# Optimization experiments

Measured on AMD Instinct MI355X. Metric: run time of the kernel, lower is better.

Reference implementation:

```python
import jax, jax.numpy as jnp
import numpy as np

B, C, H, W = 8, 3, 64, 64
HORIZON = 32
WIDTH = 32
M1 = M2 = M3 = 8
N_LAYERS = 4
C_OUT = 3


def setup_inputs() -> dict:
    key = jax.random.key(0)
    ks = jax.random.split(key, 16)
    scale = 1.0 / (WIDTH * WIDTH)
    wshape = (N_LAYERS, 4, WIDTH, WIDTH, M1, M2, M3)
    return {
        "x_t": jax.random.normal(ks[0], (B, C, H, W), dtype=jnp.float32),
        "p_w": jax.random.normal(ks[1], (WIDTH, C + 3), dtype=jnp.float32) * 0.1,
        "p_b": jnp.zeros((WIDTH,), dtype=jnp.float32),
        "spec_wr": scale * jax.random.normal(ks[2], wshape, dtype=jnp.float32),
        "spec_wi": scale * jax.random.normal(ks[3], wshape, dtype=jnp.float32),
        "pw_w": jax.random.normal(ks[4], (N_LAYERS, WIDTH, WIDTH), dtype=jnp.float32) * 0.1,
        "pw_b": jnp.zeros((N_LAYERS, WIDTH), dtype=jnp.float32),
        "q1_w": jax.random.normal(ks[5], (2 * WIDTH, WIDTH), dtype=jnp.float32) * 0.1,
        "q1_b": jnp.zeros((2 * WIDTH,), dtype=jnp.float32),
        "q2_w": jax.random.normal(ks[6], (C_OUT, 2 * WIDTH), dtype=jnp.float32) * 0.1,
        "q2_b": jnp.zeros((C_OUT,), dtype=jnp.float32),
        "horizon": HORIZON,
    }


def _conv1x1(x, w, b):
    # x: [b, i, x, y, z], w: [o, i] -> [b, o, x, y, z]
    return jnp.einsum("oi,bixyz->boxyz", w, x) + b[None, :, None, None, None]


def _spectral_conv3d(x, wr, wi):
    # x: [b, i, H, W, T]; wr/wi: [4, i, o, m1, m2, m3]
    h, w_, t = x.shape[-3], x.shape[-2], x.shape[-1]
    xf = jnp.fft.rfftn(x, axes=(-3, -2, -1))  # [b, i, H, W, T//2+1]
    wc = (wr + 1j * wi).astype(xf.dtype)
    m1 = min(M1, xf.shape[-3]); m2 = min(M2, xf.shape[-2]); m3 = min(M3, xf.shape[-1])
    mul = lambda a, ww: jnp.einsum("bixyz,ioxyz->boxyz", a, ww)
    out = jnp.zeros((x.shape[0], wr.shape[2]) + xf.shape[2:], dtype=xf.dtype)
    out = out.at[:, :, :m1, :m2, :m3].set(mul(xf[:, :, :m1, :m2, :m3], wc[0, :, :, :m1, :m2, :m3]))
    out = out.at[:, :, -m1:, :m2, :m3].set(mul(xf[:, :, -m1:, :m2, :m3], wc[1, :, :, :m1, :m2, :m3]))
    out = out.at[:, :, :m1, -m2:, :m3].set(mul(xf[:, :, :m1, -m2:, :m3], wc[2, :, :, :m1, :m2, :m3]))
    out = out.at[:, :, -m1:, -m2:, :m3].set(mul(xf[:, :, -m1:, -m2:, :m3], wc[3, :, :, :m1, :m2, :m3]))
    return jnp.fft.irfftn(out, s=(h, w_, t), axes=(-3, -2, -1))


def _grid_3d(b, h, w, t, dtype):
    gy = jnp.broadcast_to(jnp.linspace(0.0, 1.0, h, dtype=dtype)[None, None, :, None, None], (b, 1, h, w, t))
    gx = jnp.broadcast_to(jnp.linspace(0.0, 1.0, w, dtype=dtype)[None, None, None, :, None], (b, 1, h, w, t))
    gt = jnp.broadcast_to(jnp.linspace(0.0, 1.0, t, dtype=dtype)[None, None, None, None, :], (b, 1, h, w, t))
    return jnp.concatenate([gy, gx, gt], axis=1)


def reference(x_t, p_w, p_b, spec_wr, spec_wi, pw_w, pw_b, q1_w, q1_b, q2_w, q2_b, horizon):
    b, c, h, w = x_t.shape
    x = jnp.broadcast_to(x_t[..., None], (b, c, h, w, horizon))  # repeat over time
    grid = _grid_3d(b, h, w, horizon, x_t.dtype)
    x = jnp.concatenate([x, grid], axis=1)  # [b, c+3, h, w, t]
    x = _conv1x1(x, p_w, p_b)
    for l in range(N_LAYERS):
        x = jax.nn.gelu(
            _spectral_conv3d(x, spec_wr[l], spec_wi[l]) + _conv1x1(x, pw_w[l], pw_b[l]),
            approximate=False,
        )
    x = _conv1x1(x, q1_w, q1_b)
    x = jax.nn.gelu(x, approximate=False)
    x = _conv1x1(x, q2_w, q2_b)
    # [b, c_out, h, w, t] -> [b, t, c_out, h, w]
    return jnp.transpose(x, (0, 4, 1, 2, 3))
```

## Files before the change

### kernel.cpp

```cpp
#include <hip/hip_runtime.h>
#include <math.h>


#define TWO_PI 6.2831853071795864769f

typedef short bf16x8 __attribute__((ext_vector_type(8)));
typedef float f32x4 __attribute__((ext_vector_type(4)));
typedef float v2f __attribute__((ext_vector_type(2)));

__device__ __forceinline__ f32x4 mfma16(bf16x8 a, bf16x8 b, f32x4 c) {
    return __builtin_amdgcn_mfma_f32_16x16x32_bf16(a, b, c, 0, 0, 0);
}

__device__ __forceinline__ void split8(float4 a, float4 b, bf16x8& h, bf16x8& l) {
    float f[8] = {a.x, a.y, a.z, a.w, b.x, b.y, b.z, b.w};
    #pragma unroll
    for (int i = 0; i < 8; ++i) {
        unsigned u = __float_as_uint(f[i]);
        h[i] = (short)(u >> 16);
        float hf = __uint_as_float(u & 0xFFFF0000u);
        float lf = f[i] - hf;
        l[i] = (short)(__float_as_uint(lf) >> 16);
    }
}

__device__ __forceinline__ unsigned packhl(float f) {
    unsigned u = __float_as_uint(f);
    unsigned hi = u & 0xFFFF0000u;
    float lf = f - __uint_as_float(hi);
    return hi | (__float_as_uint(lf) >> 16);
}

__device__ __forceinline__ void unpack8(uint4 a, uint4 b, bf16x8& h, bf16x8& l) {
    unsigned u[8] = {a.x, a.y, a.z, a.w, b.x, b.y, b.z, b.w};
    #pragma unroll
    for (int i = 0; i < 8; ++i) {
        h[i] = (short)(u[i] >> 16);
        l[i] = (short)(u[i] & 0xFFFFu);
    }
}

__device__ __forceinline__ v2f make2(float x) { v2f r; r.x = x; r.y = x; return r; }
__device__ __forceinline__ v2f fma2(v2f a, v2f b, v2f c) { return __builtin_elementwise_fma(a, b, c); }

__device__ __forceinline__ v2f gelu2(v2f v) {
    v2f u = v * 0.70710678118654752f;
    v2f a = __builtin_elementwise_abs(u);
    v2f den = fma2(a, make2(0.3275911f), make2(1.0f));
    v2f t; t.x = __builtin_amdgcn_rcpf(den.x); t.y = __builtin_amdgcn_rcpf(den.y);
    v2f p = t * (0.254829592f + t * (-0.284496736f + t * (1.421413741f +
            t * (-1.453152027f + t * 1.061405429f))));
    v2f e; e.x = __expf(-u.x * u.x); e.y = __expf(-u.y * u.y);
    v2f m = fma2(-p, e, make2(1.0f));
    v2f erfu = __builtin_elementwise_copysign(m, u);
    return 0.5f * v * (1.0f + erfu);
}

__device__ __forceinline__ void gelu4(f32x4& q) {
    v2f p0; p0.x = q[0]; p0.y = q[1];
    v2f p1; p1.x = q[2]; p1.y = q[3];
    p0 = gelu2(p0); p1 = gelu2(p1);
    q[0] = p0.x; q[1] = p0.y; q[2] = p1.x; q[3] = p1.y;
}

__device__ __forceinline__ void make_fwd_A(int l15, int quad, bf16x8& Gh, bf16x8& Gl) {
    int k = l15 >> 1;
    float s0, c0, ds, dc;
    __sincosf((float)(k * quad * 8) * (TWO_PI / 32.0f), &s0, &c0);
    __sincosf((float)k * (TWO_PI / 32.0f), &ds, &dc);
    float m[8];
    float cc = c0, ss = s0;
    #pragma unroll
    for (int j = 0; j < 8; ++j) {
        m[j] = (l15 & 1) ? -ss : cc;
        float nc = cc * dc - ss * ds;
        float ns = ss * dc + cc * ds;
        cc = nc; ss = ns;
    }
    split8(make_float4(m[0], m[1], m[2], m[3]),
           make_float4(m[4], m[5], m[6], m[7]), Gh, Gl);
}

__device__ __forceinline__ void fwd_tdft(const unsigned* up, int b, int sp0,
                                         float2* __restrict__ T1,
                                         int wb, int l15, int quad,
                                         bf16x8 Gh, bf16x8 Gl) {
    #pragma unroll
    for (int nt = 0; nt < 4; ++nt) {
        int r = wb + nt * 16 + l15;
        const uint4* p = (const uint4*)(up + r * 36 + quad * 8);
        bf16x8 bh, bl; unpack8(p[0], p[1], bh, bl);
        f32x4 d = {0.f, 0.f, 0.f, 0.f};
        d = mfma16(Gh, bh, d);
        d = mfma16(Gl, bh, d);
        d = mfma16(Gh, bl, d);
        int c = r & 31, spl = r >> 5;
        float4* ob = (float4*)(T1 + ((long)(b * 32 + c) * 4096 + sp0 + spl) * 8 + quad * 2);
        *ob = make_float4(d[0], d[1], d[2], d[3]);
    }
}

__global__ __launch_bounds__(256) void k_lift(const float* __restrict__ xt,
                                              const float* __restrict__ pw,
                                              const float* __restrict__ pb,
                                              float* __restrict__ X,
                                              float2* __restrict__ T1) {
    __shared__ unsigned xs[9216];
    int g = blockIdx.x;
    int spt = g & 511, b = g >> 9;
    int sp0 = spt * 8;
    int y = sp0 >> 6, x0 = sp0 & 63;
    int tid = threadIdx.x;
    int t = tid & 31, spl = tid >> 5;
    int sp = sp0 + spl;
    float a0 = xt[(b * 3 + 0) * 4096 + sp];
    float a1 = xt[(b * 3 + 1) * 4096 + sp];
    float a2 = xt[(b * 3 + 2) * 4096 + sp];
    float gy = y * (1.0f / 63.0f), gx = (x0 + spl) * (1.0f / 63.0f), gt = t * (1.0f / 31.0f);
    float v[32];
    #pragma unroll
    for (int c = 0; c < 32; ++c) {
        const float* w = pw + c * 6;
        v[c] = pb[c] + w[0] * a0 + w[1] * a1 + w[2] * a2
             + w[3] * gy + w[4] * gx + w[5] * gt;
    }
    float* xg = X + (((long)(b * 4096 + sp)) * 32 + t) * 32;
    #pragma unroll
    for (int j = 0; j < 8; ++j)
        ((float4*)xg)[j] = make_float4(v[4*j], v[4*j+1], v[4*j+2], v[4*j+3]);
    #pragma unroll
    for (int c = 0; c < 32; ++c)
        xs[(spl * 32 + c) * 36 + t] = packhl(v[c]);
    int wave = tid >> 6, lane = tid & 63, l15 = lane & 15, quad = lane >> 4;
    bf16x8 Gh, Gl; make_fwd_A(l15, quad, Gh, Gl);
    __syncthreads();
    fwd_tdft(xs, b, sp0, T1, wave * 64, l15, quad, Gh, Gl);
}

__global__ __launch_bounds__(256) void k_xdft(const float2* __restrict__ T1, float2* __restrict__ T2) {
    __shared__ float2 s[1024];
    __shared__ float2 tw[64];
    int g = blockIdx.x;
    int ypair = g & 31; int bc = g >> 5;
    long base = ((long)bc * 64 + ypair * 2) * 512;
    int tid = threadIdx.x;
    for (int k = tid; k < 1024; k += 256) s[k] = T1[base + k];
    if (tid < 64) { float sn, cs; __sincosf(tid * (TWO_PI / 64.0f), &sn, &cs); tw[tid] = make_float2(cs, sn); }
    __syncthreads();
    #pragma unroll
    for (int r = 0; r < 2; ++r) {
        int j = tid + r * 256;
        int half = j >> 8, rem = j & 255;
        int idx = half * 512 + rem;
        float2 a = s[idx], b2 = s[idx + 256];
        s[idx] = make_float2(a.x + b2.x, a.y + b2.y);
        s[idx + 256] = make_float2(a.x - b2.x, a.y - b2.y);
    }
    __syncthreads();
    int half = tid >> 7, jj = tid & 127;
    int kxi = jj >> 3, kt = jj & 7;
    int kx = kxi < 8 ? kxi : kxi + 48;
    const float2* row = s + half * 512 + (kx & 1) * 256;
    float sr = 0.f, si = 0.f;
    for (int x = 0; x < 32; ++x) {
        float2 w = tw[(kx * x) & 63];
        float2 a = row[x * 8 + kt];
        sr += a.x * w.x + a.y * w.y;
        si += a.y * w.x - a.x * w.y;
    }
    T2[((long)bc * 64 + ypair * 2 + half) * 128 + jj] = make_float2(sr, si);
}

__global__ __launch_bounds__(128) void k_ydft(const float2* __restrict__ T2, float2* __restrict__ T3) {
    __shared__ float2 s[512];
    __shared__ float2 tw[64];
    int g = blockIdx.x;
    int kx = g & 15; int bc = g >> 4;
    int tid = threadIdx.x;
    for (int k = tid; k < 512; k += 128) {
        int y = k >> 3, kt = k & 7;
        s[k] = T2[((long)bc * 64 + y) * 128 + kx * 8 + kt];
    }
    if (tid < 64) { float sn, cs; __sincosf(tid * (TWO_PI / 64.0f), &sn, &cs); tw[tid] = make_float2(cs, sn); }
    __syncthreads();
    #pragma unroll
    for (int r = 0; r < 2; ++r) {
        int j = tid + r * 128;
        float2 a = s[j], b2 = s[j + 256];
        s[j] = make_float2(a.x + b2.x, a.y + b2.y);
        s[j + 256] = make_float2(a.x - b2.x, a.y - b2.y);
    }
    __syncthreads();
    int kyi = tid >> 3, kt = tid & 7;
    int ky = kyi < 8 ? kyi : kyi + 48;
    const float2* row = s + (ky & 1) * 256;
    float sr = 0.f, si = 0.f;
    for (int y = 0; y < 32; ++y) {
        float2 w = tw[(ky * y) & 63];
        float2 a = row[y * 8 + kt];
        sr += a.x * w.x + a.y * w.y;
        si += a.y * w.x - a.x * w.y;
    }
    T3[((long)bc * 256 + kyi * 16 + kx) * 8 + kt] = make_float2(sr, si);
}

__global__ __launch_bounds__(256) void k_mix2(const float2* __restrict__ T3,
                                              const float* __restrict__ wr,
                                              const float* __restrict__ wi,
                                              float2* __restrict__ T4, int layer) {
    __shared__ float2 s[2304];
    int mode = blockIdx.x;
    int kyi = mode >> 4, kxi = mode & 15;
    int tid = threadIdx.x;
    {
        int bb = tid >> 5, i = tid & 31;
        const float2* src = T3 + ((long)(bb * 32 + i) * 256 + mode) * 8;
        float2* dst = s + (i * 8 + bb) * 9;
        #pragma unroll
        for (int k = 0; k < 8; ++k) dst[k] = src[k];
    }
    __syncthreads();
    int corner = (kyi >= 8 ? 1 : 0) + (kxi >= 8 ? 2 : 0);
    long wbase = (long)(layer * 4 + corner) * 524288 + (long)(kyi & 7) * 64 + (long)(kxi & 7) * 8;
    int o = tid >> 3, kt = tid & 7;
    long wb = wbase + (long)o * 512 + kt;
    float2 acc[8];
    #pragma unroll
    for (int bb = 0; bb < 8; ++bb) acc[bb] = make_float2(0.f, 0.f);
    for (int i = 0; i < 32; ++i) {
        float r = wr[wb + (long)i * 16384], im = wi[wb + (long)i * 16384];
        #pragma unroll
        for (int bb = 0; bb < 8; ++bb) {
            float2 a = s[(i * 8 + bb) * 9 + kt];
            acc[bb].x += a.x * r - a.y * im;
            acc[bb].y += a.x * im + a.y * r;
        }
    }
    #pragma unroll
    for (int bb = 0; bb < 8; ++bb)
        T4[((long)(bb * 32 + o) * 256 + mode) * 8 + kt] = acc[bb];
}

__global__ __launch_bounds__(256) void k_invy(const float2* __restrict__ T4, float2* __restrict__ T5) {
    __shared__ float2 s[128];
    __shared__ float2 tw[64];
    __shared__ float2 pmP[56], pmM[56];
    int g = blockIdx.x;
    int kx = g & 15; int bc = g >> 4;
    int tid = threadIdx.x;
    if (tid < 128) {
        int kyi = tid >> 3, kt = tid & 7;
        s[tid] = T4[((long)bc * 256 + kyi * 16 + kx) * 8 + kt];
    } else if (tid < 192) {
        int m = tid - 128; float sn, cs; __sincosf(m * (TWO_PI / 64.0f), &sn, &cs); tw[m] = make_float2(cs, sn);
    }
    __syncthreads();
    if (tid < 56) {
        int j = (tid >> 3) + 1, kt = tid & 7;
        float2 a = s[j * 8 + kt], b2 = s[(16 - j) * 8 + kt];
        pmP[tid] = make_float2(a.x + b2.x, a.y + b2.y);
        pmM[tid] = make_float2(a.x - b2.x, a.y - b2.y);
    }
    __syncthreads();
    #pragma unroll
    for (int r = 0; r < 2; ++r) {
        int j = tid + r * 256;
        int y = j >> 3, kt = j & 7;
        float2 A0 = s[kt], A8 = s[64 + kt];
        float2 w8 = tw[(8 * y) & 63];
        float sr = A0.x + A8.x * w8.x + A8.y * w8.y;
        float si = A0.y + A8.y * w8.x - A8.x * w8.y;
        #pragma unroll
        for (int jj = 1; jj < 8; ++jj) {
            float2 w = tw[(jj * y) & 63];
            float2 P = pmP[(jj - 1) * 8 + kt], M = pmM[(jj - 1) * 8 + kt];
            sr += P.x * w.x - M.y * w.y;
            si += P.y * w.x + M.x * w.y;
        }
        T5[((long)bc * 64 + y) * 128 + kx * 8 + kt] = make_float2(sr, si);
    }
}

__global__ __launch_bounds__(256) void k_invx(const float2* __restrict__ T5, float2* __restrict__ T6) {
    __shared__ float2 s[128];
    __shared__ float2 tw[64];
    __shared__ float2 pmP[56], pmM[56];
    int g = blockIdx.x;
    int tid = threadIdx.x;
    if (tid < 128) {
        s[tid] = T5[(long)g * 128 + tid];
    } else if (tid < 192) {
        int m = tid - 128; float sn, cs; __sincosf(m * (TWO_PI / 64.0f), &sn, &cs); tw[m] = make_float2(cs, sn);
    }
    __syncthreads();
    if (tid < 56) {
        int j = (tid >> 3) + 1, kt = tid & 7;
        float2 a = s[j * 8 + kt], b2 = s[(16 - j) * 8 + kt];
        pmP[tid] = make_float2(a.x + b2.x, a.y + b2.y);
        pmM[tid] = make_float2(a.x - b2.x, a.y - b2.y);
    }
    __syncthreads();
    #pragma unroll
    for (int r = 0; r < 2; ++r) {
        int j = tid + r * 256;
        int x = j >> 3, kt = j & 7;
        float2 A0 = s[kt], A8 = s[64 + kt];
        float2 w8 = tw[(8 * x) & 63];
        float sr = A0.x + A8.x * w8.x + A8.y * w8.y;
        float si = A0.y + A8.y * w8.x - A8.x * w8.y;
        #pragma unroll
        for (int jj = 1; jj < 8; ++jj) {
            float2 w = tw[(jj * x) & 63];
            float2 P = pmP[(jj - 1) * 8 + kt], M = pmM[(jj - 1) * 8 + kt];
            sr += P.x * w.x - M.y * w.y;
            si += P.y * w.x + M.x * w.y;
        }
        T6[(long)g * 512 + j] = make_float2(sr, si);
    }
}

__device__ __forceinline__ void make_invt_A(int l15, int quad, bf16x8 Ah[2], bf16x8 Al[2]) {
    #pragma unroll
    for (int th = 0; th < 2; ++th) {
        float m[8];
        if (quad < 2) {
            int tt = th * 16 + l15;
            #pragma unroll
            for (int kk = 0; kk < 4; ++kk) {
                int k = quad * 4 + kk;
                float sn, cs;
                __sincosf((float)(k * tt) * (TWO_PI / 32.0f), &sn, &cs);
                float w = k ? 2.0f : 1.0f;
                m[2 * kk] = w * cs;
                m[2 * kk + 1] = -w * sn;
            }
        } else {
            #pragma unroll
            for (int j = 0; j < 8; ++j) m[j] = 0.f;
        }
        split8(make_float4(m[0], m[1], m[2], m[3]),
               make_float4(m[4], m[5], m[6], m[7]), Ah[th], Al[th]);
    }
}

__global__ __launch_bounds__(256) void k_fuse3(float* __restrict__ X, const float2* __restrict__ T6,
                                               const float* __restrict__ pww,
                                               const float* __restrict__ pwb,
                                               float2* __restrict__ T1, int layer) {
    __shared__ float smem[9216];
    float2* ts = (float2*)smem;
    int g = blockIdx.x;
    int spt = g & 511, b = g >> 9;
    int sp0 = spt * 8;
    int tid = threadIdx.x;
    {
        int o = tid >> 3, spl = tid & 7;
        const float4* src = (const float4*)(T6 + ((long)(b * 32 + o) * 4096 + sp0 + spl) * 8);
        float4* dst = (float4*)(ts + o * 66 + spl * 8);
        const float S = 1.0f / 131072.0f;
        #pragma unroll
        for (int j = 0; j < 4; ++j) {
            float4 q = src[j];
            dst[j] = make_float4(q.x * S, q.y * S, q.z * S, q.w * S);
        }
    }
    int wave = tid >> 6, lane = tid & 63, l15 = lane & 15, quad = lane >> 4;
    int wb = wave * 64;
    const float* wl = pww + layer * 1024;
    const float* bl = pwb + layer * 32;
    bf16x8 wah[2], wal[2];
    f32x4 acc[2][4];
    #pragma unroll
    for (int mt = 0; mt < 2; ++mt) {
        const float4* p = (const float4*)(wl + (mt * 16 + l15) * 32 + quad * 8);
        split8(p[0], p[1], wah[mt], wal[mt]);
        float4 bv = *(const float4*)(bl + mt * 16 + quad * 4);
        f32x4 bi; bi[0] = bv.x; bi[1] = bv.y; bi[2] = bv.z; bi[3] = bv.w;
        #pragma unroll
        for (int nt = 0; nt < 4; ++nt) acc[mt][nt] = bi;
    }
    #pragma unroll
    for (int nt = 0; nt < 4; ++nt) {
        int pt = wb + nt * 16 + l15;
        int spl = pt >> 5, t = pt & 31;
        const float4* xp = (const float4*)(X + (((long)(b * 4096 + sp0 + spl)) * 32 + t) * 32 + quad * 8);
        bf16x8 bh, blo; split8(xp[0], xp[1], bh, blo);
        #pragma unroll
        for (int mt = 0; mt < 2; ++mt) {
            acc[mt][nt] = mfma16(wah[mt], bh, acc[mt][nt]);
            acc[mt][nt] = mfma16(wal[mt], bh, acc[mt][nt]);
            acc[mt][nt] = mfma16(wah[mt], blo, acc[mt][nt]);
        }
    }
    bf16x8 Ah[2], Al[2];
    make_invt_A(l15, quad, Ah, Al);
    __syncthreads();
    bf16x8 Bh[2][2], Bl[2][2];
    #pragma unroll
    for (int sph = 0; sph < 2; ++sph) {
        int spl = 2 * wave + sph;
        #pragma unroll
        for (int ch = 0; ch < 2; ++ch) {
            float4 q0 = make_float4(0.f, 0.f, 0.f, 0.f), q1 = q0;
            if (quad < 2) {
                const float4* p = (const float4*)(ts + (ch * 16 + l15) * 66 + spl * 8 + quad * 4);
                q0 = p[0]; q1 = p[1];
            }
            split8(q0, q1, Bh[sph][ch], Bl[sph][ch]);
        }
    }
    __syncthreads();
    #pragma unroll
    for (int sph = 0; sph < 2; ++sph) {
        int spl = 2 * wave + sph;
        #pragma unroll
        for (int ch = 0; ch < 2; ++ch)
            #pragma unroll
            for (int th = 0; th < 2; ++th) {
                f32x4 d = {0.f, 0.f, 0.f, 0.f};
                d = mfma16(Ah[th], Bh[sph][ch], d);
                d = mfma16(Al[th], Bh[sph][ch], d);
                d = mfma16(Ah[th], Bl[sph][ch], d);
                float* wp = smem + (spl * 32 + th * 16 + quad * 4) * 36 + ch * 16 + l15;
                wp[0] = d[0]; wp[36] = d[1]; wp[72] = d[2]; wp[108] = d[3];
            }
    }
    __syncthreads();
    #pragma unroll
    for (int mt = 0; mt < 2; ++mt)
        #pragma unroll
        for (int nt = 0; nt < 4; ++nt) {
            int pt = wb + nt * 16 + l15;
            int spl = pt >> 5, t = pt & 31;
            float4 sp4 = *(const float4*)(smem + (spl * 32 + t) * 36 + mt * 16 + quad * 4);
            acc[mt][nt][0] += sp4.x; acc[mt][nt][1] += sp4.y;
            acc[mt][nt][2] += sp4.z; acc[mt][nt][3] += sp4.w;
        }
    __syncthreads();
    bf16x8 Gh, Gl; make_fwd_A(l15, quad, Gh, Gl);
    #pragma unroll
    for (int mt = 0; mt < 2; ++mt)
        #pragma unroll
        for (int nt = 0; nt < 4; ++nt) gelu4(acc[mt][nt]);
    unsigned* up = (unsigned*)smem;
    #pragma unroll
    for (int mt = 0; mt < 2; ++mt)
        #pragma unroll
        for (int nt = 0; nt < 4; ++nt) {
            int pt = wb + nt * 16 + l15;
            int spl = pt >> 5, t = pt & 31;
            int o0 = mt * 16 + quad * 4;
            float4 w4 = make_float4(acc[mt][nt][0], acc[mt][nt][1], acc[mt][nt][2], acc[mt][nt][3]);
            *(float4*)(X + (((long)(b * 4096 + sp0 + spl)) * 32 + t) * 32 + o0) = w4;
            up[(spl * 32 + o0 + 0) * 36 + t] = packhl(w4.x);
            up[(spl * 32 + o0 + 1) * 36 + t] = packhl(w4.y);
            up[(spl * 32 + o0 + 2) * 36 + t] = packhl(w4.z);
            up[(spl * 32 + o0 + 3) * 36 + t] = packhl(w4.w);
        }
    __syncthreads();
    fwd_tdft(up, b, sp0, T1, wb, l15, quad, Gh, Gl);
}

__global__ __launch_bounds__(256) void k_fuse3_last(const float* __restrict__ X, const float2* __restrict__ T6,
                                                    const float* __restrict__ pww, const float* __restrict__ pwb,
                                                    const float* __restrict__ q1w, const float* __restrict__ q1b,
                                                    const float* __restrict__ q2w, const float* __restrict__ q2b,
                                                    float* __restrict__ out) {
    __shared__ float smem[9408];
    float2* ts = (float2*)smem;
    int g = blockIdx.x;
    int spt = g & 511, b = g >> 9;
    int sp0 = spt * 8;
    int tid = threadIdx.x;
    {
        int o = tid >> 3, spl = tid & 7;
        const float4* src = (const float4*)(T6 + ((long)(b * 32 + o) * 4096 + sp0 + spl) * 8);
        float4* dst = (float4*)(ts + o * 66 + spl * 8);
        const float S = 1.0f / 131072.0f;
        #pragma unroll
        for (int j = 0; j < 4; ++j) {
            float4 q = src[j];
            dst[j] = make_float4(q.x * S, q.y * S, q.z * S, q.w * S);
        }
    }
    if (tid < 192) smem[9216 + tid] = q2w[tid];
    int wave = tid >> 6, lane = tid & 63, l15 = lane & 15, quad = lane >> 4;
    int wb = wave * 64;
    const float* wl = pww + 3 * 1024;
    const float* bl = pwb + 3 * 32;
    bf16x8 wah[2], wal[2];
    f32x4 acc[2][4];
    #pragma unroll
    for (int mt = 0; mt < 2; ++mt) {
        const float4* p = (const float4*)(wl + (mt * 16 + l15) * 32 + quad * 8);
        split8(p[0], p[1], wah[mt], wal[mt]);
        float4 bv = *(const float4*)(bl + mt * 16 + quad * 4);
        f32x4 bi; bi[0] = bv.x; bi[1] = bv.y; bi[2] = bv.z; bi[3] = bv.w;
        #pragma unroll
        for (int nt = 0; nt < 4; ++nt) acc[mt][nt] = bi;
    }
    #pragma unroll
    for (int nt = 0; nt < 4; ++nt) {
        int pt = wb + nt * 16 + l15;
        int spl = pt >> 5, t = pt & 31;
        const float4* xp = (const float4*)(X + (((long)(b * 4096 + sp0 + spl)) * 32 + t) * 32 + quad * 8);
        bf16x8 bh, blo; split8(xp[0], xp[1], bh, blo);
        #pragma unroll
        for (int mt = 0; mt < 2; ++mt) {
            acc[mt][nt] = mfma16(wah[mt], bh, acc[mt][nt]);
            acc[mt][nt] = mfma16(wal[mt], bh, acc[mt][nt]);
            acc[mt][nt] = mfma16(wah[mt], blo, acc[mt][nt]);
        }
    }
    bf16x8 Ah[2], Al[2];
    make_invt_A(l15, quad, Ah, Al);
    __syncthreads();
    bf16x8 Bh[2][2], Bl[2][2];
    #pragma unroll
    for (int sph = 0; sph < 2; ++sph) {
        int spl = 2 * wave + sph;
        #pragma unroll
        for (int ch = 0; ch < 2; ++ch) {
            float4 q0 = make_float4(0.f, 0.f, 0.f, 0.f), q1 = q0;
            if (quad < 2) {
                const float4* p = (const float4*)(ts + (ch * 16 + l15) * 66 + spl * 8 + quad * 4);
                q0 = p[0]; q1 = p[1];
            }
            split8(q0, q1, Bh[sph][ch], Bl[sph][ch]);
        }
    }
    __syncthreads();
    #pragma unroll
    for (int sph = 0; sph < 2; ++sph) {
        int spl = 2 * wave + sph;
        #pragma unroll
        for (int ch = 0; ch < 2; ++ch)
            #pragma unroll
            for (int th = 0; th < 2; ++th) {
                f32x4 d = {0.f, 0.f, 0.f, 0.f};
                d = mfma16(Ah[th], Bh[sph][ch], d);
                d = mfma16(Al[th], Bh[sph][ch], d);
                d = mfma16(Ah[th], Bl[sph][ch], d);
                float* wp = smem + (spl * 32 + th * 16 + quad * 4) * 36 + ch * 16 + l15;
                wp[0] = d[0]; wp[36] = d[1]; wp[72] = d[2]; wp[108] = d[3];
            }
    }
    __syncthreads();
    #pragma unroll
    for (int mt = 0; mt < 2; ++mt)
        #pragma unroll
        for (int nt = 0; nt < 4; ++nt) {
            int pt = wb + nt * 16 + l15;
            int spl = pt >> 5, t = pt & 31;
            float4 sp4 = *(const float4*)(smem + (spl * 32 + t) * 36 + mt * 16 + quad * 4);
            acc[mt][nt][0] += sp4.x; acc[mt][nt][1] += sp4.y;
            acc[mt][nt][2] += sp4.z; acc[mt][nt][3] += sp4.w;
        }
    #pragma unroll
    for (int mt = 0; mt < 2; ++mt)
        #pragma unroll
        for (int nt = 0; nt < 4; ++nt) gelu4(acc[mt][nt]);
    #pragma unroll
    for (int mt = 0; mt < 2; ++mt)
        #pragma unroll
        for (int nt = 0; nt < 4; ++nt) {
            int pt = wb + nt * 16 + l15;
            int o0 = mt * 16 + quad * 4;
            *(float4*)(smem + pt * 36 + o0) =
                make_float4(acc[mt][nt][0], acc[mt][nt][1], acc[mt][nt][2], acc[mt][nt][3]);
        }
    __syncthreads();
    bf16x8 qah[4], qal[4];
    f32x4 qbv[4];
    #pragma unroll
    for (int mt = 0; mt < 4; ++mt) {
        const float4* p = (const float4*)(q1w + (mt * 16 + l15) * 32 + quad * 8);
        split8(p[0], p[1], qah[mt], qal[mt]);
        float4 bv = *(const float4*)(q1b + mt * 16 + quad * 4);
        qbv[mt][0] = bv.x; qbv[mt][1] = bv.y; qbv[mt][2] = bv.z; qbv[mt][3] = bv.w;
    }
    const float* q2l = smem + 9216;
    float q2b0 = q2b[0], q2b1 = q2b[1], q2b2 = q2b[2];
    float oc0[4], oc1[4], oc2[4];
    #pragma unroll
    for (int nt = 0; nt < 4; ++nt) {
        int pt = wb + nt * 16 + l15;
        const float4* bp = (const float4*)(smem + pt * 36 + quad * 8);
        bf16x8 bh, blo; split8(bp[0], bp[1], bh, blo);
        float p0 = 0.f, p1 = 0.f, p2 = 0.f;
        #pragma unroll
        for (int mt = 0; mt < 4; ++mt) {
            f32x4 h = qbv[mt];
            h = mfma16(qah[mt], bh, h);
            h = mfma16(qal[mt], bh, h);
            h = mfma16(qah[mt], blo, h);
            gelu4(h);
            #pragma unroll
            for (int reg = 0; reg < 4; ++reg) {
                int hh = mt * 16 + quad * 4 + reg;
                p0 += q2l[hh] * h[reg];
                p1 += q2l[64 + hh] * h[reg];
                p2 += q2l[128 + hh] * h[reg];
            }
        }
        p0 += __shfl_xor(p0, 16); p0 += __shfl_xor(p0, 32);
        p1 += __shfl_xor(p1, 16); p1 += __shfl_xor(p1, 32);
        p2 += __shfl_xor(p2, 16); p2 += __shfl_xor(p2, 32);
        oc0[nt] = p0 + q2b0; oc1[nt] = p1 + q2b1; oc2[nt] = p2 + q2b2;
    }
    __syncthreads();
    if (quad == 0) {
        #pragma unroll
        for (int nt = 0; nt < 4; ++nt) {
            int pt = wb + nt * 16 + l15;
            int spl = pt >> 5, t = pt & 31;
            smem[(t * 3 + 0) * 9 + spl] = oc0[nt];
            smem[(t * 3 + 1) * 9 + spl] = oc1[nt];
            smem[(t * 3 + 2) * 9 + spl] = oc2[nt];
        }
    }
    __syncthreads();
    for (int m = tid; m < 768; m += 256) {
        int u = m >> 3, spl = m & 7;
        out[((long)(b * 96 + u)) * 4096 + sp0 + spl] = smem[u * 9 + spl];
    }
}

extern "C" void kernel_launch(void* const* d_in, const int* in_sizes, int n_in,
                              void* d_out, int out_size, void* d_ws, size_t ws_size,
                              hipStream_t stream) {
    const float* xt  = (const float*)d_in[0];
    const float* pw  = (const float*)d_in[1];
    const float* pb  = (const float*)d_in[2];
    const float* swr = (const float*)d_in[3];
    const float* swi = (const float*)d_in[4];
    const float* pww = (const float*)d_in[5];
    const float* pwb = (const float*)d_in[6];
    const float* q1w = (const float*)d_in[7];
    const float* q1b = (const float*)d_in[8];
    const float* q2w = (const float*)d_in[9];
    const float* q2b = (const float*)d_in[10];
    float* out = (float*)d_out;

    float*  X  = (float*)d_ws;
    float2* T1 = (float2*)(X + 33554432);
    float2* T2 = (float2*)((float*)T1 + 16777216);
    float2* T3 = (float2*)((float*)T2 + 4194304);
    float2* T4 = (float2*)((float*)T3 + 1048576);

    k_lift<<<4096, 256, 0, stream>>>(xt, pw, pb, X, T1);
    for (int l = 0; l < 4; ++l) {
        k_xdft<<<8192, 256, 0, stream>>>(T1, T2);
        k_ydft<<<4096, 128, 0, stream>>>(T2, T3);
        k_mix2<<<256, 256, 0, stream>>>(T3, swr, swi, T4, l);
        k_invy<<<4096, 256, 0, stream>>>(T4, T2);
        k_invx<<<16384, 256, 0, stream>>>(T2, T1);
        if (l < 3)
            k_fuse3<<<4096, 256, 0, stream>>>(X, T1, pww, pwb, T1, l);
        else
            k_fuse3_last<<<4096, 256, 0, stream>>>(X, T1, pww, pwb, q1w, q1b, q2w, q2b, out);
    }
}
```

Before: 787.1 us.

## Fuse inverse x-DFT into fuse3 kernels via bf16-split MFMA

Removes the separate k_invx kernel and performs the inverse DFT along x inside k_fuse3 and k_fuse3_last. Each block stages the T5 row for its y in two channel halves through shared memory and computes the 8 spatial points with MFMA, using a twiddle matrix split into bf16 hi/lo parts that also folds in the normalisation scale. This avoids writing and re-reading the full-resolution T6 intermediate and saves one launch per layer. In exchange, each block redundantly transforms a 64-point row to produce only 8 outputs, adds extra barriers, and uses a split-bf16 precision path.

```diff
diff --git a/kernel.cpp b/kernel.cpp
--- a/kernel.cpp
+++ b/kernel.cpp
@@ -97,6 +97,63 @@
         int c = r & 31, spl = r >> 5;
         float4* ob = (float4*)(T1 + ((long)(b * 32 + c) * 4096 + sp0 + spl) * 8 + quad * 2);
         *ob = make_float4(d[0], d[1], d[2], d[3]);
+    }
+}
+
+__device__ __forceinline__ void make_invx_A(int x0, int l15, int quad, bf16x8& Ah, bf16x8& Al) {
+    int spl = l15 >> 1, ro = l15 & 1;
+    float xx = (float)(x0 + spl);
+    const float S = 1.0f / 131072.0f;
+    float f[8];
+    #pragma unroll
+    for (int m = 0; m < 4; ++m) {
+        int kxi = quad * 4 + m;
+        float kx = (float)(kxi < 8 ? kxi : kxi - 16);
+        float sn, cs;
+        __sincosf(kx * xx * (TWO_PI / 64.0f), &sn, &cs);
+        f[2 * m]     = ro ? S * sn : S * cs;
+        f[2 * m + 1] = ro ? S * cs : -S * sn;
+    }
+    split8(make_float4(f[0], f[1], f[2], f[3]),
+           make_float4(f[4], f[5], f[6], f[7]), Ah, Al);
+}
+
+__device__ __forceinline__ void stage_T5_half(const float2* __restrict__ T5, float* smem,
+                                              int b, int y, int half, int tid) {
+    float2* T5h = (float2*)(smem + 4224);
+    int c = tid >> 4, q4 = tid & 15;
+    const float4* src = (const float4*)(T5 + ((long)((b * 32 + half * 16 + c) * 64 + y)) * 128);
+    float4* dst = (float4*)(T5h + c * 130);
+    #pragma unroll
+    for (int j = 0; j < 4; ++j) dst[q4 + j * 16] = src[q4 + j * 16];
+}
+
+__device__ __forceinline__ void invx_half(float* smem, int half, int wave, int l15, int quad,
+                                          bf16x8 xAh, bf16x8 xAl) {
+    const float2* T5h = (const float2*)(smem + 4224);
+    #pragma unroll
+    for (int nt2 = 0; nt2 < 2; ++nt2) {
+        int tile = wave * 2 + nt2;
+        int ol = tile * 2 + (l15 >> 3), kt = l15 & 7;
+        float f[8];
+        #pragma unroll
+        for (int m = 0; m < 4; ++m) {
+            float2 v = T5h[ol * 130 + (quad * 4 + m) * 8 + kt];
+            f[2 * m] = v.x; f[2 * m + 1] = v.y;
+        }
+        bf16x8 bh, bl;
+        split8(make_float4(f[0], f[1], f[2], f[3]),
+               make_float4(f[4], f[5], f[6], f[7]), bh, bl);
+        f32x4 d = {0.f, 0.f, 0.f, 0.f};
+        d = mfma16(xAh, bh, d);
+        d = mfma16(xAl, bh, d);
+        d = mfma16(xAh, bl, d);
+        int o = half * 16 + ol;
+        #pragma unroll
+        for (int reg = 0; reg < 4; ++reg) {
+            int m_ = quad * 4 + reg, spl = m_ >> 1, ri = m_ & 1;
+            smem[o * 132 + spl * 16 + kt * 2 + ri] = d[reg];
+        }
     }
 }
 
@@ -281,44 +338,6 @@
     }
 }
 
-__global__ __launch_bounds__(256) void k_invx(const float2* __restrict__ T5, float2* __restrict__ T6) {
-    __shared__ float2 s[128];
-    __shared__ float2 tw[64];
-    __shared__ float2 pmP[56], pmM[56];
-    int g = blockIdx.x;
-    int tid = threadIdx.x;
-    if (tid < 128) {
-        s[tid] = T5[(long)g * 128 + tid];
-    } else if (tid < 192) {
-        int m = tid - 128; float sn, cs; __sincosf(m * (TWO_PI / 64.0f), &sn, &cs); tw[m] = make_float2(cs, sn);
-    }
-    __syncthreads();
-    if (tid < 56) {
-        int j = (tid >> 3) + 1, kt = tid & 7;
-        float2 a = s[j * 8 + kt], b2 = s[(16 - j) * 8 + kt];
-        pmP[tid] = make_float2(a.x + b2.x, a.y + b2.y);
-        pmM[tid] = make_float2(a.x - b2.x, a.y - b2.y);
-    }
-    __syncthreads();
-    #pragma unroll
-    for (int r = 0; r < 2; ++r) {
-        int j = tid + r * 256;
-        int x = j >> 3, kt = j & 7;
-        float2 A0 = s[kt], A8 = s[64 + kt];
-        float2 w8 = tw[(8 * x) & 63];
-        float sr = A0.x + A8.x * w8.x + A8.y * w8.y;
-        float si = A0.y + A8.y * w8.x - A8.x * w8.y;
-        #pragma unroll
-        for (int jj = 1; jj < 8; ++jj) {
-            float2 w = tw[(jj * x) & 63];
-            float2 P = pmP[(jj - 1) * 8 + kt], M = pmM[(jj - 1) * 8 + kt];
-            sr += P.x * w.x - M.y * w.y;
-            si += P.y * w.x + M.x * w.y;
-        }
-        T6[(long)g * 512 + j] = make_float2(sr, si);
-    }
-}
-
 __device__ __forceinline__ void make_invt_A(int l15, int quad, bf16x8 Ah[2], bf16x8 Al[2]) {
     #pragma unroll
     for (int th = 0; th < 2; ++th) {
@@ -343,29 +362,19 @@
     }
 }
 
-__global__ __launch_bounds__(256) void k_fuse3(float* __restrict__ X, const float2* __restrict__ T6,
+__global__ __launch_bounds__(256) void k_fuse3(float* __restrict__ X, const float2* __restrict__ T5,
                                                const float* __restrict__ pww,
                                                const float* __restrict__ pwb,
                                                float2* __restrict__ T1, int layer) {
     __shared__ float smem[9216];
-    float2* ts = (float2*)smem;
     int g = blockIdx.x;
     int spt = g & 511, b = g >> 9;
     int sp0 = spt * 8;
+    int y = sp0 >> 6, x0 = sp0 & 63;
     int tid = threadIdx.x;
-    {
-        int o = tid >> 3, spl = tid & 7;
-        const float4* src = (const float4*)(T6 + ((long)(b * 32 + o) * 4096 + sp0 + spl) * 8);
-        float4* dst = (float4*)(ts + o * 66 + spl * 8);
-        const float S = 1.0f / 131072.0f;
-        #pragma unroll
-        for (int j = 0; j < 4; ++j) {
-            float4 q = src[j];
-            dst[j] = make_float4(q.x * S, q.y * S, q.z * S, q.w * S);
-        }
-    }
     int wave = tid >> 6, lane = tid & 63, l15 = lane & 15, quad = lane >> 4;
     int wb = wave * 64;
+    stage_T5_half(T5, smem, b, y, 0, tid);
     const float* wl = pww + layer * 1024;
     const float* bl = pwb + layer * 32;
     bf16x8 wah[2], wal[2];
@@ -394,7 +403,16 @@
     }
     bf16x8 Ah[2], Al[2];
     make_invt_A(l15, quad, Ah, Al);
-    __syncthreads();
+    bf16x8 xAh, xAl;
+    make_invx_A(x0, l15, quad, xAh, xAl);
+    __syncthreads();
+    invx_half(smem, 0, wave, l15, quad, xAh, xAl);
+    __syncthreads();
+    stage_T5_half(T5, smem, b, y, 1, tid);
+    __syncthreads();
+    invx_half(smem, 1, wave, l15, quad, xAh, xAl);
+    __syncthreads();
+    float2* ts = (float2*)smem;
     bf16x8 Bh[2][2], Bl[2][2];
     #pragma unroll
     for (int sph = 0; sph < 2; ++sph) {
@@ -461,31 +479,21 @@
     fwd_tdft(up, b, sp0, T1, wb, l15, quad, Gh, Gl);
 }
 
-__global__ __launch_bounds__(256) void k_fuse3_last(const float* __restrict__ X, const float2* __restrict__ T6,
+__global__ __launch_bounds__(256) void k_fuse3_last(const float* __restrict__ X, const float2* __restrict__ T5,
                                                     const float* __restrict__ pww, const float* __restrict__ pwb,
                                                     const float* __restrict__ q1w, const float* __restrict__ q1b,
                                                     const float* __restrict__ q2w, const float* __restrict__ q2b,
                                                     float* __restrict__ out) {
     __shared__ float smem[9408];
-    float2* ts = (float2*)smem;
     int g = blockIdx.x;
     int spt = g & 511, b = g >> 9;
     int sp0 = spt * 8;
+    int y = sp0 >> 6, x0 = sp0 & 63;
     int tid = threadIdx.x;
-    {
-        int o = tid >> 3, spl = tid & 7;
-        const float4* src = (const float4*)(T6 + ((long)(b * 32 + o) * 4096 + sp0 + spl) * 8);
-        float4* dst = (float4*)(ts + o * 66 + spl * 8);
-        const float S = 1.0f / 131072.0f;
-        #pragma unroll
-        for (int j = 0; j < 4; ++j) {
-            float4 q = src[j];
-            dst[j] = make_float4(q.x * S, q.y * S, q.z * S, q.w * S);
-        }
-    }
-    if (tid < 192) smem[9216 + tid] = q2w[tid];
     int wave = tid >> 6, lane = tid & 63, l15 = lane & 15, quad = lane >> 4;
     int wb = wave * 64;
+    stage_T5_half(T5, smem, b, y, 0, tid);
+    if (tid < 192) smem[9216 + tid] = q2w[tid];
     const float* wl = pww + 3 * 1024;
     const float* bl = pwb + 3 * 32;
     bf16x8 wah[2], wal[2];
@@ -514,7 +522,16 @@
     }
     bf16x8 Ah[2], Al[2];
     make_invt_A(l15, quad, Ah, Al);
-    __syncthreads();
+    bf16x8 xAh, xAl;
+    make_invx_A(x0, l15, quad, xAh, xAl);
+    __syncthreads();
+    invx_half(smem, 0, wave, l15, quad, xAh, xAl);
+    __syncthreads();
+    stage_T5_half(T5, smem, b, y, 1, tid);
+    __syncthreads();
+    invx_half(smem, 1, wave, l15, quad, xAh, xAl);
+    __syncthreads();
+    float2* ts = (float2*)smem;
     bf16x8 Bh[2][2], Bl[2][2];
     #pragma unroll
     for (int sph = 0; sph < 2; ++sph) {
@@ -654,10 +671,9 @@
         k_ydft<<<4096, 128, 0, stream>>>(T2, T3);
         k_mix2<<<256, 256, 0, stream>>>(T3, swr, swi, T4, l);
         k_invy<<<4096, 256, 0, stream>>>(T4, T2);
-        k_invx<<<16384, 256, 0, stream>>>(T2, T1);
         if (l < 3)
-            k_fuse3<<<4096, 256, 0, stream>>>(X, T1, pww, pwb, T1, l);
+            k_fuse3<<<4096, 256, 0, stream>>>(X, T2, pww, pwb, T1, l);
         else
-            k_fuse3_last<<<4096, 256, 0, stream>>>(X, T1, pww, pwb, q1w, q1b, q2w, q2b, out);
-    }
-}
+            k_fuse3_last<<<4096, 256, 0, stream>>>(X, T2, pww, pwb, q1w, q1b, q2w, q2b, out);
+    }
+}
```

Result: faster. 754.8 us (-4.1%).
